# Performance work log

Measured on AMD Instinct MI355X. Metric: run time of the kernel, lower is better.

## Reference

```python
import jax, jax.numpy as jnp
import numpy as np

T, B, I, H = 256, 128, 512, 1024

def setup_inputs() -> dict:
    key = jax.random.key(0)
    k1, k2, k3, k4, k5 = jax.random.split(key, 5)
    s_ih = 1.0 / np.sqrt(H)
    return {
        "x": jax.random.normal(k1, (T, B, I), dtype=jnp.float32),
        "hidden": jnp.zeros((B, H), dtype=jnp.float32),
        "W_ih": jax.random.uniform(k2, (H, I), jnp.float32, -s_ih, s_ih),
        "W_hh": jax.random.uniform(k3, (H, H), jnp.float32, -s_ih, s_ih),
        "b_ih": jax.random.uniform(k4, (H,), jnp.float32, -s_ih, s_ih),
        "b_hh": jax.random.uniform(k5, (H,), jnp.float32, -s_ih, s_ih),
    }

def reference(x, hidden, W_ih, W_hh, b_ih, b_hh):
    # Faithful to the source: forward() applies the RNNCell to the SAME
    # initial hidden at every timestep (hidden is never updated in the loop).
    # out[t] = relu(x[t] @ W_ih^T + b_ih + hidden @ W_hh^T + b_hh)
    h_term = hidden @ W_hh.T + b_hh          # (B, H), shared across time
    pre = jnp.einsum('tbi,hi->tbh', x, W_ih) + b_ih + h_term  # (T, B, H)
    out = jax.nn.relu(pre)
    return out, out[-1]
```

## Files before the change

### kernel.cpp

```cpp
#include <hip/hip_runtime.h>
#include <hip/hip_bf16.h>
#include <stdint.h>

#define T_DIM 256
#define B_DIM 128
#define I_DIM 512
#define H_DIM 1024
#define M_DIM (T_DIM * B_DIM)

#define PACK_BLOCKS (264 * 8192 / 256)
#define BIAS_BLOCKS 512

typedef __attribute__((ext_vector_type(4))) float f32x4;
typedef __attribute__((ext_vector_type(8))) short short8;

__device__ inline unsigned short f2bf(float f) {
    __hip_bfloat16 h = __float2bfloat16(f);
    unsigned short u;
    __builtin_memcpy(&u, &h, sizeof(u));
    return u;
}

__device__ inline void gload_lds16(const void* g, void* l) {
    __builtin_amdgcn_global_load_lds(
        (const __attribute__((address_space(1))) uint32_t*)g,
        (__attribute__((address_space(3))) uint32_t*)l, 16, 0, 0);
}

template <bool WITH_PACK>
__global__ __launch_bounds__(256) void prep(
    const float* __restrict__ x, const float* __restrict__ W_ih,
    unsigned short* __restrict__ Xp,
    const float* __restrict__ hidden, const float* __restrict__ W_hh,
    const float* __restrict__ b_ih, const float* __restrict__ b_hh,
    float* __restrict__ biasall) {
    const int bid = blockIdx.x;
    const int tid = threadIdx.x;

    if (WITH_PACK && bid < PACK_BLOCKS) {
        int id = bid * 256 + tid;
        int slot = id & 7;
        int row = (id >> 3) & 127;
        int kst = (id >> 10) & 7;
        int tile = id >> 13;
        int g = slot ^ (row & 7);
        const float* base = (tile < 256)
                                ? (x + (size_t)tile * 128 * I_DIM)
                                : (W_ih + (size_t)(tile - 256) * 128 * I_DIM);
        const float* s = base + (size_t)row * I_DIM + kst * 64 + g * 8;
        f32x4 lo = *(const f32x4*)s;
        f32x4 hi = *(const f32x4*)(s + 4);
        union { unsigned short us[8]; short8 v; } pk;
#pragma unroll
        for (int j = 0; j < 4; ++j) {
            pk.us[j] = f2bf(lo[j]);
            pk.us[4 + j] = f2bf(hi[j]);
        }
        *(short8*)(Xp + (size_t)id * 8) = pk.v;
        return;
    }

    const int pbase = WITH_PACK ? PACK_BLOCKS : 0;
    const int gw = (bid - pbase) * 4 + (tid >> 6);
    const int lane = tid & 63;
    const int h0 = (gw >> 3) * 4;
    const int b0 = (gw & 7) * 16;

    f32x4 wreg[4][4];
#pragma unroll
    for (int hh = 0; hh < 4; ++hh)
#pragma unroll
        for (int it = 0; it < 4; ++it)
            wreg[hh][it] = *(const f32x4*)(W_hh + (size_t)(h0 + hh) * H_DIM +
                                           it * 256 + lane * 4);
    float bias2[4];
#pragma unroll
    for (int hh = 0; hh < 4; ++hh) bias2[hh] = b_ih[h0 + hh] + b_hh[h0 + hh];

#pragma unroll
    for (int b = 0; b < 16; ++b) {
        f32x4 hreg[4];
#pragma unroll
        for (int it = 0; it < 4; ++it)
            hreg[it] = *(const f32x4*)(hidden + (size_t)(b0 + b) * H_DIM +
                                       it * 256 + lane * 4);
        float s[4] = {0.f, 0.f, 0.f, 0.f};
#pragma unroll
        for (int hh = 0; hh < 4; ++hh)
#pragma unroll
            for (int it = 0; it < 4; ++it)
#pragma unroll
                for (int j = 0; j < 4; ++j)
                    s[hh] += wreg[hh][it][j] * hreg[it][j];
#pragma unroll
        for (int m = 1; m < 64; m <<= 1)
#pragma unroll
            for (int hh = 0; hh < 4; ++hh) s[hh] += __shfl_xor(s[hh], m, 64);
        if (lane == 0) {
#pragma unroll
            for (int hh = 0; hh < 4; ++hh)
                biasall[(size_t)(b0 + b) * H_DIM + h0 + hh] = s[hh] + bias2[hh];
        }
    }
}

__global__ __launch_bounds__(256, 3) void gemm64(
    const unsigned short* __restrict__ Xp, const unsigned short* __restrict__ Wp,
    const float* __restrict__ biasall, float* __restrict__ C,
    float* __restrict__ Clast) {
    __shared__ unsigned short As[2][64 * 64];
    __shared__ unsigned short Bs[2][128 * 64];

    const int tid = threadIdx.x;
    const int lane = tid & 63;
    const int wid = tid >> 6;
    const int wm = wid >> 1, wn = wid & 1;
    const int llo = lane & 15, lhi = lane >> 4;

    const int orig = blockIdx.x;
    const int wg = (orig & 7) * 512 + (orig >> 3);
    const int mt = wg >> 3;
    const int nt = wg & 7;
    const int m0 = mt * 64, n0 = nt * 128;

    const unsigned short* Abase =
        Xp + (size_t)(mt >> 1) * 65536 + (size_t)(mt & 1) * 4096 + (size_t)tid * 8;
    const unsigned short* Bbase = Wp + (size_t)nt * 65536 + (size_t)tid * 8;

    auto stage = [&](int kst, int buf) {
        const unsigned short* a = Abase + (size_t)kst * 8192;
        const unsigned short* b = Bbase + (size_t)kst * 8192;
        gload_lds16(a, (char*)As[buf] + tid * 16);
        gload_lds16(a + 2048, (char*)As[buf] + 4096 + tid * 16);
#pragma unroll
        for (int g = 0; g < 4; ++g)
            gload_lds16(b + g * 2048, (char*)Bs[buf] + (g * 256 + tid) * 16);
    };

    f32x4 acc[2][4] = {};

    auto compute = [&](int buf) {
#pragma unroll
        for (int ks = 0; ks < 2; ++ks) {
            short8 af[2], bfv[4];
#pragma unroll
            for (int mi = 0; mi < 2; ++mi) {
                int ar = wm * 32 + mi * 16 + llo;
                int slot = ((ks << 2) + lhi) ^ (ar & 7);
                af[mi] = *(const short8*)&As[buf][ar * 64 + slot * 8];
            }
#pragma unroll
            for (int ni = 0; ni < 4; ++ni) {
                int br = wn * 64 + ni * 16 + llo;
                int slot = ((ks << 2) + lhi) ^ (br & 7);
                bfv[ni] = *(const short8*)&Bs[buf][br * 64 + slot * 8];
            }
#pragma unroll
            for (int mi = 0; mi < 2; ++mi)
#pragma unroll
                for (int ni = 0; ni < 4; ++ni)
                    acc[mi][ni] = __builtin_amdgcn_mfma_f32_16x16x32_bf16(
                        af[mi], bfv[ni], acc[mi][ni], 0, 0, 0);
        }
    };

    stage(0, 0);
    stage(1, 1);
#pragma unroll
    for (int kt = 0; kt < 8; ++kt) {
        const int buf = kt & 1;
        if (kt < 7)
            asm volatile("s_waitcnt vmcnt(6)" ::: "memory");
        else
            asm volatile("s_waitcnt vmcnt(0)" ::: "memory");
        __builtin_amdgcn_s_barrier();
        __builtin_amdgcn_sched_barrier(0);
        compute(buf);
        __builtin_amdgcn_sched_barrier(0);
        __builtin_amdgcn_s_barrier();
        if (kt + 2 < 8) stage(kt + 2, buf);
    }

    const bool last_tiles = (mt >= 510);
#pragma unroll
    for (int mi = 0; mi < 2; ++mi) {
#pragma unroll
        for (int ni = 0; ni < 4; ++ni) {
            int col = n0 + wn * 64 + ni * 16 + llo;
            int rowb = m0 + wm * 32 + mi * 16 + lhi * 4;
#pragma unroll
            for (int r = 0; r < 4; ++r) {
                int row = rowb + r;
                float v = acc[mi][ni][r] + biasall[(row & 127) * H_DIM + col];
                v = fmaxf(v, 0.0f);
                C[(size_t)row * H_DIM + col] = v;
                if (last_tiles) Clast[(row & 127) * H_DIM + col] = v;
            }
        }
    }
}

__global__ __launch_bounds__(256, 2) void gemm_bt(
    const float* __restrict__ A, const float* __restrict__ Bm,
    int M, int N, int K, const float* __restrict__ bias0,
    float* __restrict__ C, float* __restrict__ Clast) {
    __shared__ unsigned short As[128 * 64];
    __shared__ unsigned short Bs[128 * 64];
    const int tid = threadIdx.x;
    const int wid = tid >> 6, lane = tid & 63;
    const int wr = wid >> 1, wc = wid & 1;
    const int lhi = lane >> 4, llo = lane & 15;
    const int orig = blockIdx.x, nwg = gridDim.x;
    const int wg = (nwg > 8 && (nwg & 7) == 0)
                       ? ((orig & 7) * (nwg >> 3) + (orig >> 3)) : orig;
    const int m0 = (wg >> 3) * 128, n0 = (wg & 7) * 128;
    const int srow = tid >> 3, c8 = tid & 7;
    const int slot8 = (c8 ^ (srow & 7)) * 8;
    const float* Aptr = A + (size_t)(m0 + srow) * K + c8 * 8;
    const float* Bptr = Bm + (size_t)(n0 + srow) * K + c8 * 8;
    f32x4 pf[2][4][2];
    auto issue = [&](int k0) {
#pragma unroll
        for (int g = 0; g < 4; ++g) {
            const float* pa = Aptr + (size_t)g * 32 * K + k0;
            const float* pb = Bptr + (size_t)g * 32 * K + k0;
            pf[0][g][0] = *(const f32x4*)pa; pf[0][g][1] = *(const f32x4*)(pa + 4);
            pf[1][g][0] = *(const f32x4*)pb; pf[1][g][1] = *(const f32x4*)(pb + 4);
        }
    };
    auto write_lds = [&]() {
#pragma unroll
        for (int g = 0; g < 4; ++g) {
            union { unsigned short s[8]; short8 v; } pka, pkb;
#pragma unroll
            for (int j = 0; j < 4; ++j) {
                pka.s[j] = f2bf(pf[0][g][0][j]); pka.s[4 + j] = f2bf(pf[0][g][1][j]);
                pkb.s[j] = f2bf(pf[1][g][0][j]); pkb.s[4 + j] = f2bf(pf[1][g][1][j]);
            }
            *(short8*)&As[(srow + g * 32) * 64 + slot8] = pka.v;
            *(short8*)&Bs[(srow + g * 32) * 64 + slot8] = pkb.v;
        }
    };
    f32x4 acc[4][4] = {};
    auto compute = [&]() {
#pragma unroll
        for (int ks = 0; ks < 2; ++ks) {
            short8 afr[4], bfr[4];
#pragma unroll
            for (int mi = 0; mi < 4; ++mi) {
                int ar = wr * 64 + mi * 16 + llo;
                afr[mi] = *(const short8*)&As[ar * 64 + (((ks << 2) + lhi) ^ (ar & 7)) * 8];
            }
#pragma unroll
            for (int ni = 0; ni < 4; ++ni) {
                int br = wc * 64 + ni * 16 + llo;
                bfr[ni] = *(const short8*)&Bs[br * 64 + (((ks << 2) + lhi) ^ (br & 7)) * 8];
            }
#pragma unroll
            for (int mi = 0; mi < 4; ++mi)
#pragma unroll
                for (int ni = 0; ni < 4; ++ni)
                    acc[mi][ni] = __builtin_amdgcn_mfma_f32_16x16x32_bf16(
                        afr[mi], bfr[ni], acc[mi][ni], 0, 0, 0);
        }
    };
    issue(0); write_lds(); __syncthreads();
    for (int k0 = 64; k0 < K; k0 += 64) {
        issue(k0); compute(); __syncthreads(); write_lds(); __syncthreads();
    }
    compute();
    const bool last_tile = (m0 == M - 128);
#pragma unroll
    for (int mi = 0; mi < 4; ++mi)
#pragma unroll
        for (int ni = 0; ni < 4; ++ni) {
            int col = n0 + wc * 64 + ni * 16 + llo;
            int rowb = m0 + wr * 64 + mi * 16 + lhi * 4;
#pragma unroll
            for (int r = 0; r < 4; ++r) {
                int row = rowb + r;
                float v = fmaxf(acc[mi][ni][r] + bias0[(row & 127) * N + col], 0.f);
                C[(size_t)row * N + col] = v;
                if (last_tile) Clast[(row & 127) * N + col] = v;
            }
        }
}

extern "C" void kernel_launch(void* const* d_in, const int* in_sizes, int n_in,
                              void* d_out, int out_size, void* d_ws, size_t ws_size,
                              hipStream_t stream) {
    const float* x = (const float*)d_in[0];
    const float* hidden = (const float*)d_in[1];
    const float* W_ih = (const float*)d_in[2];
    const float* W_hh = (const float*)d_in[3];
    const float* b_ih = (const float*)d_in[4];
    const float* b_hh = (const float*)d_in[5];

    float* out = (float*)d_out;
    float* out_last = out + (size_t)T_DIM * B_DIM * H_DIM;

    float* biasall = (float*)d_ws;
    unsigned short* Xp = (unsigned short*)((char*)d_ws + 512 * 1024);
    unsigned short* Wp = Xp + (size_t)256 * 65536;
    const size_t ws_need = 512 * 1024 + (size_t)264 * 65536 * 2;

    if (ws_size >= ws_need) {
        prep<true><<<dim3(PACK_BLOCKS + BIAS_BLOCKS), dim3(256), 0, stream>>>(
            x, W_ih, Xp, hidden, W_hh, b_ih, b_hh, biasall);
        gemm64<<<dim3(4096), dim3(256), 0, stream>>>(Xp, Wp, biasall, out, out_last);
    } else {
        prep<false><<<dim3(BIAS_BLOCKS), dim3(256), 0, stream>>>(
            x, W_ih, nullptr, hidden, W_hh, b_ih, b_hh, biasall);
        gemm_bt<<<dim3(M_DIM / 128 * (H_DIM / 128)), dim3(256), 0, stream>>>(
            x, W_ih, M_DIM, H_DIM, I_DIM, biasall, out, out_last);
    }
}
```

Baseline: 117.2 us.

## Load fp32 activations directly in GEMM and convert to bf16 in registers

Removes the separate pre-pass that packed x into a bf16 workspace. The GEMM now loads fp32 rows of x straight into registers, double-buffered across k-steps, and converts them to bf16 MFMA operands in registers, so A no longer goes through LDS. Only W_ih is still pre-packed. This avoids writing and re-reading the packed activation copy, at the cost of more VGPR use and in-loop conversion work. It also raises wave priority around the MFMA section with s_setprio.

```diff
diff --git a/kernel.cpp b/kernel.cpp
--- a/kernel.cpp
+++ b/kernel.cpp
@@ -8,7 +8,7 @@
 #define H_DIM 1024
 #define M_DIM (T_DIM * B_DIM)
 
-#define PACK_BLOCKS (264 * 8192 / 256)
+#define WPACK_BLOCKS 256
 #define BIAS_BLOCKS 512
 
 typedef __attribute__((ext_vector_type(4))) float f32x4;
@@ -27,41 +27,39 @@
         (__attribute__((address_space(3))) uint32_t*)l, 16, 0, 0);
 }
 
-template <bool WITH_PACK>
+template <int N>
+__device__ inline void vwait() {
+    if constexpr (N == 0)       asm volatile("s_waitcnt vmcnt(0)" ::: "memory");
+    else if constexpr (N == 4)  asm volatile("s_waitcnt vmcnt(4)" ::: "memory");
+    else                        asm volatile("s_waitcnt vmcnt(12)" ::: "memory");
+}
+
 __global__ __launch_bounds__(256) void prep(
-    const float* __restrict__ x, const float* __restrict__ W_ih,
-    unsigned short* __restrict__ Xp,
+    const float* __restrict__ W_ih, unsigned short* __restrict__ Wp,
     const float* __restrict__ hidden, const float* __restrict__ W_hh,
     const float* __restrict__ b_ih, const float* __restrict__ b_hh,
     float* __restrict__ biasall) {
     const int bid = blockIdx.x;
     const int tid = threadIdx.x;
 
-    if (WITH_PACK && bid < PACK_BLOCKS) {
+    if (bid < WPACK_BLOCKS) {
         int id = bid * 256 + tid;
         int slot = id & 7;
         int row = (id >> 3) & 127;
         int kst = (id >> 10) & 7;
-        int tile = id >> 13;
+        int wt = id >> 13;
         int g = slot ^ (row & 7);
-        const float* base = (tile < 256)
-                                ? (x + (size_t)tile * 128 * I_DIM)
-                                : (W_ih + (size_t)(tile - 256) * 128 * I_DIM);
-        const float* s = base + (size_t)row * I_DIM + kst * 64 + g * 8;
+        const float* s = W_ih + (size_t)(wt * 128 + row) * I_DIM + kst * 64 + g * 8;
         f32x4 lo = *(const f32x4*)s;
         f32x4 hi = *(const f32x4*)(s + 4);
         union { unsigned short us[8]; short8 v; } pk;
 #pragma unroll
-        for (int j = 0; j < 4; ++j) {
-            pk.us[j] = f2bf(lo[j]);
-            pk.us[4 + j] = f2bf(hi[j]);
-        }
-        *(short8*)(Xp + (size_t)id * 8) = pk.v;
+        for (int j = 0; j < 4; ++j) { pk.us[j] = f2bf(lo[j]); pk.us[4 + j] = f2bf(hi[j]); }
+        *(short8*)(Wp + (size_t)id * 8) = pk.v;
         return;
     }
 
-    const int pbase = WITH_PACK ? PACK_BLOCKS : 0;
-    const int gw = (bid - pbase) * 4 + (tid >> 6);
+    const int gw = (bid - WPACK_BLOCKS) * 4 + (tid >> 6);
     const int lane = tid & 63;
     const int h0 = (gw >> 3) * 4;
     const int b0 = (gw & 7) * 16;
@@ -90,8 +88,7 @@
 #pragma unroll
             for (int it = 0; it < 4; ++it)
 #pragma unroll
-                for (int j = 0; j < 4; ++j)
-                    s[hh] += wreg[hh][it][j] * hreg[it][j];
+                for (int j = 0; j < 4; ++j) s[hh] += wreg[hh][it][j] * hreg[it][j];
 #pragma unroll
         for (int m = 1; m < 64; m <<= 1)
 #pragma unroll
@@ -104,11 +101,10 @@
     }
 }
 
-__global__ __launch_bounds__(256, 3) void gemm64(
-    const unsigned short* __restrict__ Xp, const unsigned short* __restrict__ Wp,
+__global__ __launch_bounds__(256, 3) void gemm_dra(
+    const float* __restrict__ X, const unsigned short* __restrict__ Wp,
     const float* __restrict__ biasall, float* __restrict__ C,
     float* __restrict__ Clast) {
-    __shared__ unsigned short As[2][64 * 64];
     __shared__ unsigned short Bs[2][128 * 64];
 
     const int tid = threadIdx.x;
@@ -123,32 +119,51 @@
     const int nt = wg & 7;
     const int m0 = mt * 64, n0 = nt * 128;
 
-    const unsigned short* Abase =
-        Xp + (size_t)(mt >> 1) * 65536 + (size_t)(mt & 1) * 4096 + (size_t)tid * 8;
+    const float* aB0 = X + (size_t)(m0 + wm * 32 + llo) * I_DIM + lhi * 8;
+    const float* aB1 = aB0 + (size_t)16 * I_DIM;
     const unsigned short* Bbase = Wp + (size_t)nt * 65536 + (size_t)tid * 8;
 
-    auto stage = [&](int kst, int buf) {
-        const unsigned short* a = Abase + (size_t)kst * 8192;
-        const unsigned short* b = Bbase + (size_t)kst * 8192;
-        gload_lds16(a, (char*)As[buf] + tid * 16);
-        gload_lds16(a + 2048, (char*)As[buf] + 4096 + tid * 16);
+    f32x4 pfa[2][2][2], pfb[2][2][2];
+    short8 af[2][2];
+
+    auto issueA = [&](int kt, f32x4 (&set)[2][2][2]) {
+#pragma unroll
+        for (int mi = 0; mi < 2; ++mi)
+#pragma unroll
+            for (int ks = 0; ks < 2; ++ks) {
+                const float* p = (mi ? aB1 : aB0) + kt * 64 + ks * 32;
+                set[mi][ks][0] = *(const f32x4*)p;
+                set[mi][ks][1] = *(const f32x4*)(p + 4);
+            }
+    };
+    auto cvtA = [&](f32x4 (&set)[2][2][2]) {
+#pragma unroll
+        for (int mi = 0; mi < 2; ++mi)
+#pragma unroll
+            for (int ks = 0; ks < 2; ++ks) {
+                union { unsigned short us[8]; short8 v; } pk;
+#pragma unroll
+                for (int j = 0; j < 4; ++j) {
+                    pk.us[j] = f2bf(set[mi][ks][0][j]);
+                    pk.us[4 + j] = f2bf(set[mi][ks][1][j]);
+                }
+                af[mi][ks] = pk.v;
+            }
+    };
+    auto issueB = [&](int kst, int buf) {
 #pragma unroll
         for (int g = 0; g < 4; ++g)
-            gload_lds16(b + g * 2048, (char*)Bs[buf] + (g * 256 + tid) * 16);
+            gload_lds16(Bbase + kst * 8192 + g * 2048,
+                        (char*)Bs[buf] + (g * 256 + tid) * 16);
     };
 
     f32x4 acc[2][4] = {};
 
     auto compute = [&](int buf) {
+        __builtin_amdgcn_s_setprio(1);
 #pragma unroll
         for (int ks = 0; ks < 2; ++ks) {
-            short8 af[2], bfv[4];
-#pragma unroll
-            for (int mi = 0; mi < 2; ++mi) {
-                int ar = wm * 32 + mi * 16 + llo;
-                int slot = ((ks << 2) + lhi) ^ (ar & 7);
-                af[mi] = *(const short8*)&As[buf][ar * 64 + slot * 8];
-            }
+            short8 bfv[4];
 #pragma unroll
             for (int ni = 0; ni < 4; ++ni) {
                 int br = wn * 64 + ni * 16 + llo;
@@ -160,25 +175,29 @@
 #pragma unroll
                 for (int ni = 0; ni < 4; ++ni)
                     acc[mi][ni] = __builtin_amdgcn_mfma_f32_16x16x32_bf16(
-                        af[mi], bfv[ni], acc[mi][ni], 0, 0, 0);
-        }
-    };
-
-    stage(0, 0);
-    stage(1, 1);
+                        af[mi][ks], bfv[ni], acc[mi][ni], 0, 0, 0);
+        }
+        __builtin_amdgcn_s_setprio(0);
+    };
+
+    issueA(0, pfa);
+    issueA(1, pfb);
+    issueB(0, 0);
+    issueB(1, 1);
+
 #pragma unroll
     for (int kt = 0; kt < 8; ++kt) {
-        const int buf = kt & 1;
-        if (kt < 7)
-            asm volatile("s_waitcnt vmcnt(6)" ::: "memory");
-        else
-            asm volatile("s_waitcnt vmcnt(0)" ::: "memory");
+        if (kt == 0)      vwait<4>();
+        else if (kt < 7)  vwait<12>();
+        else              vwait<0>();
+        if (kt & 1) cvtA(pfb); else cvtA(pfa);
+        if (kt + 2 < 8) { if (kt & 1) issueA(kt + 2, pfb); else issueA(kt + 2, pfa); }
         __builtin_amdgcn_s_barrier();
         __builtin_amdgcn_sched_barrier(0);
-        compute(buf);
+        compute(kt & 1);
         __builtin_amdgcn_sched_barrier(0);
         __builtin_amdgcn_s_barrier();
-        if (kt + 2 < 8) stage(kt + 2, buf);
+        if (kt + 2 < 8) issueB(kt + 2, kt & 1);
     }
 
     const bool last_tiles = (mt >= 510);
@@ -300,17 +319,16 @@
     float* out_last = out + (size_t)T_DIM * B_DIM * H_DIM;
 
     float* biasall = (float*)d_ws;
-    unsigned short* Xp = (unsigned short*)((char*)d_ws + 512 * 1024);
-    unsigned short* Wp = Xp + (size_t)256 * 65536;
-    const size_t ws_need = 512 * 1024 + (size_t)264 * 65536 * 2;
+    unsigned short* Wp = (unsigned short*)((char*)d_ws + 512 * 1024);
+    const size_t ws_need = 512 * 1024 + (size_t)H_DIM * I_DIM * 2;
 
     if (ws_size >= ws_need) {
-        prep<true><<<dim3(PACK_BLOCKS + BIAS_BLOCKS), dim3(256), 0, stream>>>(
-            x, W_ih, Xp, hidden, W_hh, b_ih, b_hh, biasall);
-        gemm64<<<dim3(4096), dim3(256), 0, stream>>>(Xp, Wp, biasall, out, out_last);
+        prep<<<dim3(WPACK_BLOCKS + BIAS_BLOCKS), dim3(256), 0, stream>>>(
+            W_ih, Wp, hidden, W_hh, b_ih, b_hh, biasall);
+        gemm_dra<<<dim3(4096), dim3(256), 0, stream>>>(x, Wp, biasall, out, out_last);
     } else {
-        prep<false><<<dim3(BIAS_BLOCKS), dim3(256), 0, stream>>>(
-            x, W_ih, nullptr, hidden, W_hh, b_ih, b_hh, biasall);
+        prep<<<dim3(WPACK_BLOCKS + BIAS_BLOCKS), dim3(256), 0, stream>>>(
+            W_ih, (unsigned short*)d_ws, hidden, W_hh, b_ih, b_hh, biasall);
         gemm_bt<<<dim3(M_DIM / 128 * (H_DIM / 128)), dim3(256), 0, stream>>>(
             x, W_ih, M_DIM, H_DIM, I_DIM, biasall, out, out_last);
     }
```

After: 177.7 us. 1.52x slower.
